# Optimization experiments

Hardware: AMD Instinct MI355X
Metric: run time of the kernel (lower is better)

Reference implementation:

```python
import jax, jax.numpy as jnp
import numpy as np

B, P, D, H, A, C = 256, 512, 16, 256, 8, 2
HID = 256
IN_MLP = H + A + 1  # 265


def setup_inputs() -> dict:
    key = jax.random.key(0)
    ks = jax.random.split(key, 12)
    s = 0.05  # small init for recurrent stability
    return {
        "particles": jax.random.normal(ks[0], (B, P, D), jnp.float32),
        "weights": jax.random.uniform(ks[1], (B, P), jnp.float32),
        "actions": jax.random.normal(ks[2], (B, A), jnp.float32),
        "time": jax.random.uniform(ks[3], (B,), jnp.float32) * 100.0,
        "Wi": jax.random.normal(ks[4], (D + 1, 3 * H), jnp.float32) * s,
        "bi": jnp.zeros((3 * H,), jnp.float32),
        "Wh_rz": jax.random.normal(ks[5], (H, 2 * H), jnp.float32) * s,
        "Wh_n": jax.random.normal(ks[6], (H, H), jnp.float32) * s,
        "bn": jnp.zeros((H,), jnp.float32),
        "mlp_W1": jax.random.normal(ks[7], (C, IN_MLP, HID), jnp.float32) * s,
        "mlp_b1": jnp.zeros((C, HID), jnp.float32),
        "mlp_W2": jax.random.normal(ks[8], (C, HID, HID), jnp.float32) * s,
        "mlp_b2": jnp.zeros((C, HID), jnp.float32),
        "mlp_W3": jax.random.normal(ks[9], (C, HID, 1), jnp.float32) * s,
        "mlp_b3": jnp.zeros((C, 1), jnp.float32),
        "num_time_steps": 100,
    }


def reference(particles, weights, actions, time, Wi, bi, Wh_rz, Wh_n, bn,
              mlp_W1, mlp_b1, mlp_W2, mlp_b2, mlp_W3, mlp_b3, num_time_steps):
    # feature_fn = identity; append weights as an extra feature channel
    x = jnp.concatenate([particles, weights[..., None]], axis=-1)  # [B, P, D+1]
    xs = jnp.swapaxes(x, 0, 1)  # [P, B, D+1], scan over particle axis

    def gru_step(h, xt):
        gi = xt @ Wi + bi  # [B, 3H]
        i_r, i_z, i_n = jnp.split(gi, 3, axis=-1)
        hrz = h @ Wh_rz  # [B, 2H], no bias (flax GRUCell hidden r/z dense)
        r = jax.nn.sigmoid(i_r + hrz[:, :H])
        z = jax.nn.sigmoid(i_z + hrz[:, H:])
        n = jnp.tanh(i_n + r * (h @ Wh_n + bn))
        h_new = (1.0 - z) * n + z * h
        return h_new, None

    h0 = jnp.zeros((particles.shape[0], H), particles.dtype)
    enc, _ = jax.lax.scan(gru_step, h0, xs)  # last hidden == take(outputs, -1, axis=-2)

    norm_time = time / num_time_steps
    hidden = jnp.concatenate([enc, actions, norm_time[..., None]], axis=-1)  # [B, IN_MLP]

    # n_critics MLPs evaluated batched over critic axis c
    h1 = jax.nn.relu(jnp.einsum('bi,cio->bco', hidden, mlp_W1) + mlp_b1)
    h2 = jax.nn.relu(jnp.einsum('bci,cio->bco', h1, mlp_W2) + mlp_b2)
    q = jnp.einsum('bci,cio->bco', h2, mlp_W3) + mlp_b3  # [B, C, 1]
    return q[..., 0]  # [B, C]
```

## Files before the change

### kernel.cpp

```cpp
#include <hip/hip_runtime.h>
#include <hip/hip_fp16.h>

typedef _Float16 h2v __attribute__((ext_vector_type(2)));
typedef _Float16 f16x8 __attribute__((ext_vector_type(8)));
typedef float f32x4 __attribute__((ext_vector_type(4)));
typedef unsigned int u32;
typedef unsigned short u16;

#define NB 256
#define NP 512
#define NH 256
#define NCOL 768

#define OFF_WH 0
#define LEN_WH 98304
#define OFF_WI (OFF_WH + LEN_WH)
#define LEN_WI 6912
#define OFF_W1 (OFF_WI + LEN_WI)
#define LEN_W1 68096
#define OFF_W2 (OFF_W1 + LEN_W1)
#define LEN_W2 65536
#define OFF_W3 (OFF_W2 + LEN_W2)
#define LEN_W3 256
#define WS_DWORDS (OFF_W3 + LEN_W3)

__device__ __forceinline__ u32 pack2(float lo, float hi) {
    h2v v; v.x = (_Float16)lo; v.y = (_Float16)hi;
    return __builtin_bit_cast(u32, v);
}

__device__ __forceinline__ float fdot2(u32 a, u32 b, float c) {
#if __has_builtin(__builtin_amdgcn_fdot2)
    return __builtin_amdgcn_fdot2(__builtin_bit_cast(h2v, a),
                                  __builtin_bit_cast(h2v, b), c, false);
#else
    h2v x = __builtin_bit_cast(h2v, a), y = __builtin_bit_cast(h2v, b);
    return c + (float)x.x * (float)y.x + (float)x.y * (float)y.y;
#endif
}

__global__ __launch_bounds__(256) void pack_kernel(
    const float* __restrict__ Wi, const float* __restrict__ Whrz,
    const float* __restrict__ Whn, const float* __restrict__ W1,
    const float* __restrict__ W2, const float* __restrict__ W3,
    u32* __restrict__ ws)
{
    for (int F = blockIdx.x * 256 + threadIdx.x; F < WS_DWORDS; F += gridDim.x * 256) {
        u32 val;
        if (F < OFF_WI) {
            int d = F & 3; int r = F >> 2;
            int l = r & 63; int q = r >> 6;
            int f = q % 48; int w = q / 48;
            int t = f >> 3; int kt = f & 7;
            int k = kt * 32 + ((l >> 4) << 3) + 2 * d;
            int col = w * 96 + t * 16 + (l & 15);
            float lo, hi;
            if (col < 512) { lo = Whrz[k * 512 + col]; hi = Whrz[(k + 1) * 512 + col]; }
            else { lo = Whn[k * 256 + (col - 512)]; hi = Whn[(k + 1) * 256 + (col - 512)]; }
            val = pack2(lo, hi);
        } else if (F < OFF_W1) {
            int j = F - OFF_WI; int kk = j / NCOL; int col = j % NCOL;
            int k = 2 * kk;
            float lo = Wi[k * NCOL + col];
            float hi = (k + 1 < 17) ? Wi[(k + 1) * NCOL + col] : 0.f;
            val = pack2(lo, hi);
        } else if (F < OFF_W2) {
            int j = F - OFF_W1; int c = j / (133 * 256); int r = j % (133 * 256);
            int kk = r >> 8; int o = r & 255;
            int k = 2 * kk;
            float lo = W1[(c * 265 + k) * 256 + o];
            float hi = (k + 1 < 265) ? W1[(c * 265 + k + 1) * 256 + o] : 0.f;
            val = pack2(lo, hi);
        } else if (F < OFF_W3) {
            int j = F - OFF_W2; int c = j >> 15; int r = j & 32767;
            int kk = r >> 8; int o = r & 255;
            float lo = W2[(c * 256 + 2 * kk) * 256 + o];
            float hi = W2[(c * 256 + 2 * kk + 1) * 256 + o];
            val = pack2(lo, hi);
        } else {
            int j = F - OFF_W3; int c = j >> 7; int jj = j & 127;
            float lo = W3[c * 256 + 2 * jj];
            float hi = W3[c * 256 + 2 * jj + 1];
            val = pack2(lo, hi);
        }
        ws[F] = val;
    }
}

__global__ __launch_bounds__(512, 2) void qnet_kernel(
    const float* __restrict__ particles, const float* __restrict__ pweights,
    const float* __restrict__ actions, const float* __restrict__ timev,
    const float* __restrict__ bi, const float* __restrict__ bn,
    const float* __restrict__ b1, const float* __restrict__ b2,
    const float* __restrict__ b3, const int* __restrict__ nts,
    const u32* __restrict__ ws, float* __restrict__ out)
{
    __shared__ __align__(16) u32 sWi[LEN_WI];
    __shared__ __align__(16) u32 sX[NP * 9];
    __shared__ __align__(16) float sCols[NCOL];
    __shared__ __align__(16) u32 sH2[NH / 2];
    __shared__ __align__(16) float sHf[NH];
    __shared__ __align__(16) float sMisc[16];

    u32* sHid = sWi;
    u16* sL1 = (u16*)sX;
    u16* sL2 = (u16*)sCols;

    const int b = blockIdx.x;
    const int tid = threadIdx.x;
    const int lane = tid & 63;
    const int wid = tid >> 6;

    f16x8 bf[48];
    {
        const uint4* gp = (const uint4*)(ws + OFF_WH) + (wid * 48) * 64 + lane;
        #pragma unroll
        for (int i = 0; i < 48; ++i) bf[i] = __builtin_bit_cast(f16x8, gp[i * 64]);
    }
    for (int j = tid; j < LEN_WI; j += 512) sWi[j] = ws[OFF_WI + j];
    {
        const float4* pr = (const float4*)(particles + (long)b * NP * 16);
        for (int j = tid; j < NP * 4; j += 512) {
            float4 v = pr[j];
            int p = j >> 2, d4 = j & 3;
            sX[p * 9 + d4 * 2]     = pack2(v.x, v.y);
            sX[p * 9 + d4 * 2 + 1] = pack2(v.z, v.w);
        }
        const float* wr = pweights + (long)b * NP;
        for (int p = tid; p < NP; p += 512) sX[p * 9 + 8] = pack2(wr[p], 0.f);
    }
    if (tid < NH / 2) sH2[tid] = 0u;
    if (tid < 8) sMisc[tid] = actions[b * 8 + tid];
    if (tid == 8) sMisc[8] = timev[b] / (float)nts[0];

    float hreg = 0.f, bir = 0.f, biz = 0.f, binn = 0.f, bnn = 0.f;
    if (tid < NH) {
        bir = bi[tid]; biz = bi[NH + tid]; binn = bi[2 * NH + tid]; bnn = bn[tid];
    }
    __syncthreads();

    const uint4* h4 = ((const uint4*)sH2) + (lane >> 4);
    float* colp = sCols + wid * 96 + (lane & 15);

    #pragma unroll 1
    for (int p = 0; p < NP; ++p) {
        f32x4 a0 = {0.f, 0.f, 0.f, 0.f}, a1 = a0, a2 = a0, a3 = a0, a4 = a0, a5 = a0;
        #pragma unroll
        for (int kt = 0; kt < 8; ++kt) {
            f16x8 av = __builtin_bit_cast(f16x8, h4[kt * 4]);
            a0 = __builtin_amdgcn_mfma_f32_16x16x32_f16(av, bf[kt],      a0, 0, 0, 0);
            a1 = __builtin_amdgcn_mfma_f32_16x16x32_f16(av, bf[8 + kt],  a1, 0, 0, 0);
            a2 = __builtin_amdgcn_mfma_f32_16x16x32_f16(av, bf[16 + kt], a2, 0, 0, 0);
            a3 = __builtin_amdgcn_mfma_f32_16x16x32_f16(av, bf[24 + kt], a3, 0, 0, 0);
            a4 = __builtin_amdgcn_mfma_f32_16x16x32_f16(av, bf[32 + kt], a4, 0, 0, 0);
            a5 = __builtin_amdgcn_mfma_f32_16x16x32_f16(av, bf[40 + kt], a5, 0, 0, 0);
        }

        float xr = 0.f, xz = 0.f, xn = 0.f;
        if (tid < NH) {
            xr = bir; xz = biz; xn = binn;
            const u32* xp = &sX[p * 9];
            #pragma unroll
            for (int kk = 0; kk < 9; ++kk) {
                u32 xv = xp[kk];
                xr = fdot2(sWi[kk * NCOL + tid], xv, xr);
                xz = fdot2(sWi[kk * NCOL + NH + tid], xv, xz);
                xn = fdot2(sWi[kk * NCOL + 2 * NH + tid], xv, xn);
            }
        }

        if (lane < 16) {
            colp[0]  = a0[0]; colp[16] = a1[0]; colp[32] = a2[0];
            colp[48] = a3[0]; colp[64] = a4[0]; colp[80] = a5[0];
        }
        __syncthreads();
        if (tid < NH) {
            float sr = sCols[tid];
            float sz = sCols[NH + tid];
            float sn = sCols[2 * NH + tid];
            float r = 1.f / (1.f + __expf(-(sr + xr)));
            float z = 1.f / (1.f + __expf(-(sz + xz)));
            float targ = xn + r * (sn + bnn);
            float e2 = __expf(2.f * targ);
            float n = 1.f - 2.f / (e2 + 1.f);
            hreg = (1.f - z) * n + z * hreg;
            _Float16 hh = (_Float16)hreg;
            ((u16*)sH2)[tid] = __builtin_bit_cast(u16, hh);
        }
        __syncthreads();
    }

    if (tid < NH) sHf[tid] = hreg;
    __syncthreads();
    if (tid < 128) sHid[tid] = pack2(sHf[2 * tid], sHf[2 * tid + 1]);
    else if (tid < 132) { int i = tid - 128; sHid[tid] = pack2(sMisc[2 * i], sMisc[2 * i + 1]); }
    else if (tid == 132) sHid[132] = pack2(sMisc[8], 0.f);
    __syncthreads();
    {
        int c = tid >> 8, o = tid & 255;
        float acc = b1[c * 256 + o];
        const u32* wp = ws + OFF_W1 + c * 133 * 256 + o;
        #pragma unroll 4
        for (int kk = 0; kk < 133; ++kk) acc = fdot2(wp[kk * 256], sHid[kk], acc);
        acc = fmaxf(acc, 0.f);
        _Float16 a16 = (_Float16)acc;
        sL1[tid] = __builtin_bit_cast(u16, a16);
    }
    __syncthreads();
    {
        int c = tid >> 8, o = tid & 255;
        float acc = b2[c * 256 + o];
        const u32* wp = ws + OFF_W2 + c * 128 * 256 + o;
        const u32* hp = (const u32*)sL1 + c * 128;
        #pragma unroll 4
        for (int kk = 0; kk < 128; ++kk) acc = fdot2(wp[kk * 256], hp[kk], acc);
        acc = fmaxf(acc, 0.f);
        _Float16 a16 = (_Float16)acc;
        sL2[tid] = __builtin_bit_cast(u16, a16);
    }
    __syncthreads();
    if (tid < 128) {
        int c = tid >> 6, l = tid & 63;
        const u32* wp = ws + OFF_W3 + c * 128;
        const u32* hp = (const u32*)sL2 + c * 128;
        float acc = fdot2(wp[l], hp[l], 0.f);
        acc = fdot2(wp[64 + l], hp[64 + l], acc);
        #pragma unroll
        for (int off = 32; off > 0; off >>= 1) acc += __shfl_down(acc, off);
        if (l == 0) out[b * 2 + c] = acc + b3[c];
    }
}

extern "C" void kernel_launch(void* const* d_in, const int* in_sizes, int n_in,
                              void* d_out, int out_size, void* d_ws, size_t ws_size,
                              hipStream_t stream) {
    const float* particles = (const float*)d_in[0];
    const float* pweights  = (const float*)d_in[1];
    const float* actions   = (const float*)d_in[2];
    const float* timev     = (const float*)d_in[3];
    const float* Wi        = (const float*)d_in[4];
    const float* bi        = (const float*)d_in[5];
    const float* Whrz      = (const float*)d_in[6];
    const float* Whn       = (const float*)d_in[7];
    const float* bn        = (const float*)d_in[8];
    const float* W1        = (const float*)d_in[9];
    const float* b1        = (const float*)d_in[10];
    const float* W2        = (const float*)d_in[11];
    const float* b2        = (const float*)d_in[12];
    const float* W3        = (const float*)d_in[13];
    const float* b3        = (const float*)d_in[14];
    const int*   nts       = (const int*)d_in[15];
    u32* ws = (u32*)d_ws;
    float* outp = (float*)d_out;

    pack_kernel<<<WS_DWORDS / 256, 256, 0, stream>>>(Wi, Whrz, Whn, W1, W2, W3, ws);
    qnet_kernel<<<NB, 512, 0, stream>>>(particles, pweights, actions, timev,
                                        bi, bn, b1, b2, b3, nts, ws, outp);
}
```

Before: 697.2 us.

## Batch input projection via MFMA every 16 steps and cut per-step barriers

The input projection x@Wi is now computed with MFMA for 16 particles at once and staged in shared memory, replacing the per-step fdot2 loop over sWi. The hidden-weight column layout is reordered so each wave owns 32 hidden units across r/z/n, letting lanes combine gates from their own MFMA accumulators without the sCols round trip. The hidden state is double-buffered, so each step needs one barrier instead of two. In exchange there is an extra barrier every 16 steps, more shared memory for sG, and only half of each wave's lanes do the gate math.

```diff
diff --git a/kernel.cpp b/kernel.cpp
--- a/kernel.cpp
+++ b/kernel.cpp
@@ -10,13 +10,12 @@
 #define NB 256
 #define NP 512
 #define NH 256
-#define NCOL 768
 
 #define OFF_WH 0
 #define LEN_WH 98304
-#define OFF_WI (OFF_WH + LEN_WH)
-#define LEN_WI 6912
-#define OFF_W1 (OFF_WI + LEN_WI)
+#define OFF_WIB (OFF_WH + LEN_WH)
+#define LEN_WIB 12288
+#define OFF_W1 (OFF_WIB + LEN_WIB)
 #define LEN_W1 68096
 #define OFF_W2 (OFF_W1 + LEN_W1)
 #define LEN_W2 65536
@@ -47,22 +46,28 @@
 {
     for (int F = blockIdx.x * 256 + threadIdx.x; F < WS_DWORDS; F += gridDim.x * 256) {
         u32 val;
-        if (F < OFF_WI) {
+        if (F < OFF_WIB) {
             int d = F & 3; int r = F >> 2;
             int l = r & 63; int q = r >> 6;
             int f = q % 48; int w = q / 48;
             int t = f >> 3; int kt = f & 7;
+            int g = t >> 1, c = t & 1;
             int k = kt * 32 + ((l >> 4) << 3) + 2 * d;
-            int col = w * 96 + t * 16 + (l & 15);
+            int col = g * 256 + w * 32 + c * 16 + (l & 15);
             float lo, hi;
             if (col < 512) { lo = Whrz[k * 512 + col]; hi = Whrz[(k + 1) * 512 + col]; }
             else { lo = Whn[k * 256 + (col - 512)]; hi = Whn[(k + 1) * 256 + (col - 512)]; }
             val = pack2(lo, hi);
         } else if (F < OFF_W1) {
-            int j = F - OFF_WI; int kk = j / NCOL; int col = j % NCOL;
-            int k = 2 * kk;
-            float lo = Wi[k * NCOL + col];
-            float hi = (k + 1 < 17) ? Wi[(k + 1) * NCOL + col] : 0.f;
+            int j = F - OFF_WIB;
+            int d = j & 3; int r = j >> 2;
+            int l = r & 63; int q = r >> 6;
+            int t = q % 6; int w = q / 6;
+            int g = t >> 1, c = t & 1;
+            int k = ((l >> 4) << 3) + 2 * d;
+            int col = g * 256 + w * 32 + c * 16 + (l & 15);
+            float lo = (k < 17) ? Wi[k * 768 + col] : 0.f;
+            float hi = (k + 1 < 17) ? Wi[(k + 1) * 768 + col] : 0.f;
             val = pack2(lo, hi);
         } else if (F < OFF_W2) {
             int j = F - OFF_W1; int c = j / (133 * 256); int r = j % (133 * 256);
@@ -95,103 +100,119 @@
     const float* __restrict__ b3, const int* __restrict__ nts,
     const u32* __restrict__ ws, float* __restrict__ out)
 {
-    __shared__ __align__(16) u32 sWi[LEN_WI];
-    __shared__ __align__(16) u32 sX[NP * 9];
-    __shared__ __align__(16) float sCols[NCOL];
-    __shared__ __align__(16) u32 sH2[NH / 2];
+    __shared__ __align__(16) u32 sX[NP * 16];
+    __shared__ __align__(16) float sG[8 * 1536];
+    __shared__ __align__(16) u32 sH2[2][128];
     __shared__ __align__(16) float sHf[NH];
     __shared__ __align__(16) float sMisc[16];
-
-    u32* sHid = sWi;
-    u16* sL1 = (u16*)sX;
-    u16* sL2 = (u16*)sCols;
 
     const int b = blockIdx.x;
     const int tid = threadIdx.x;
     const int lane = tid & 63;
     const int wid = tid >> 6;
 
-    f16x8 bf[48];
+    f16x8 bfh[48];
     {
         const uint4* gp = (const uint4*)(ws + OFF_WH) + (wid * 48) * 64 + lane;
         #pragma unroll
-        for (int i = 0; i < 48; ++i) bf[i] = __builtin_bit_cast(f16x8, gp[i * 64]);
-    }
-    for (int j = tid; j < LEN_WI; j += 512) sWi[j] = ws[OFF_WI + j];
-    {
-        const float4* pr = (const float4*)(particles + (long)b * NP * 16);
-        for (int j = tid; j < NP * 4; j += 512) {
-            float4 v = pr[j];
-            int p = j >> 2, d4 = j & 3;
-            sX[p * 9 + d4 * 2]     = pack2(v.x, v.y);
-            sX[p * 9 + d4 * 2 + 1] = pack2(v.z, v.w);
+        for (int i = 0; i < 48; ++i) bfh[i] = __builtin_bit_cast(f16x8, gp[i * 64]);
+    }
+    {
+        const float2* pr2 = (const float2*)(particles + (long)b * NP * 16);
+        for (int j = tid; j < NP * 8; j += 512) {
+            int p = j >> 3, q = j & 7;
+            float2 v = pr2[j];
+            sX[p * 16 + q] = pack2(v.x, v.y);
         }
         const float* wr = pweights + (long)b * NP;
-        for (int p = tid; p < NP; p += 512) sX[p * 9 + 8] = pack2(wr[p], 0.f);
-    }
-    if (tid < NH / 2) sH2[tid] = 0u;
+        for (int j = tid; j < NP * 8; j += 512) {
+            int p = j >> 3, q = j & 7;
+            sX[p * 16 + 8 + q] = (q == 0) ? pack2(wr[p], 0.f) : 0u;
+        }
+    }
+    if (tid < 256) ((u32*)sH2)[tid] = 0u;
     if (tid < 8) sMisc[tid] = actions[b * 8 + tid];
     if (tid == 8) sMisc[8] = timev[b] / (float)nts[0];
 
-    float hreg = 0.f, bir = 0.f, biz = 0.f, binn = 0.f, bnn = 0.f;
-    if (tid < NH) {
-        bir = bi[tid]; biz = bi[NH + tid]; binn = bi[2 * NH + tid]; bnn = bn[tid];
-    }
-    __syncthreads();
-
-    const uint4* h4 = ((const uint4*)sH2) + (lane >> 4);
-    float* colp = sCols + wid * 96 + (lane & 15);
+    float birL = 0.f, bizL = 0.f, binnL = 0.f, bnnL = 0.f, hreg = 0.f;
+    if (lane < 32) {
+        int j = wid * 32 + lane;
+        birL = bi[j]; bizL = bi[NH + j]; binnL = bi[2 * NH + j]; bnnL = bn[j];
+    }
+    __syncthreads();
+
+    const uint4* wibp = (const uint4*)(ws + OFF_WIB) + (wid * 6) * 64 + lane;
 
     #pragma unroll 1
     for (int p = 0; p < NP; ++p) {
+        if ((p & 15) == 0) {
+            f16x8 av = __builtin_bit_cast(f16x8,
+                ((const uint4*)sX)[(p + (lane & 15)) * 4 + (lane >> 4)]);
+            f32x4 z4 = {0.f, 0.f, 0.f, 0.f};
+            f32x4 g0 = __builtin_amdgcn_mfma_f32_16x16x32_f16(av, __builtin_bit_cast(f16x8, wibp[0 * 64]), z4, 0, 0, 0);
+            f32x4 g1 = __builtin_amdgcn_mfma_f32_16x16x32_f16(av, __builtin_bit_cast(f16x8, wibp[1 * 64]), z4, 0, 0, 0);
+            f32x4 g2 = __builtin_amdgcn_mfma_f32_16x16x32_f16(av, __builtin_bit_cast(f16x8, wibp[2 * 64]), z4, 0, 0, 0);
+            f32x4 g3 = __builtin_amdgcn_mfma_f32_16x16x32_f16(av, __builtin_bit_cast(f16x8, wibp[3 * 64]), z4, 0, 0, 0);
+            f32x4 g4 = __builtin_amdgcn_mfma_f32_16x16x32_f16(av, __builtin_bit_cast(f16x8, wibp[4 * 64]), z4, 0, 0, 0);
+            f32x4 g5 = __builtin_amdgcn_mfma_f32_16x16x32_f16(av, __builtin_bit_cast(f16x8, wibp[5 * 64]), z4, 0, 0, 0);
+            int sb = (lane >> 4) << 2;
+            float* gw = sG + wid * 1536 + (lane & 15);
+            #pragma unroll
+            for (int r = 0; r < 4; ++r) {
+                gw[(sb + r) * 32]          = g0[r];
+                gw[(sb + r) * 32 + 16]     = g1[r];
+                gw[512 + (sb + r) * 32]    = g2[r];
+                gw[512 + (sb + r) * 32 + 16] = g3[r];
+                gw[1024 + (sb + r) * 32]   = g4[r];
+                gw[1024 + (sb + r) * 32 + 16] = g5[r];
+            }
+            __syncthreads();
+        }
+
+        float gR = 0.f, gZ = 0.f, gN = 0.f;
+        {
+            const float* gp = sG + wid * 1536 + (p & 15) * 32 + (lane & 31);
+            gR = gp[0]; gZ = gp[512]; gN = gp[1024];
+        }
+
+        const u32* hbuf = sH2[p & 1];
         f32x4 a0 = {0.f, 0.f, 0.f, 0.f}, a1 = a0, a2 = a0, a3 = a0, a4 = a0, a5 = a0;
         #pragma unroll
         for (int kt = 0; kt < 8; ++kt) {
-            f16x8 av = __builtin_bit_cast(f16x8, h4[kt * 4]);
-            a0 = __builtin_amdgcn_mfma_f32_16x16x32_f16(av, bf[kt],      a0, 0, 0, 0);
-            a1 = __builtin_amdgcn_mfma_f32_16x16x32_f16(av, bf[8 + kt],  a1, 0, 0, 0);
-            a2 = __builtin_amdgcn_mfma_f32_16x16x32_f16(av, bf[16 + kt], a2, 0, 0, 0);
-            a3 = __builtin_amdgcn_mfma_f32_16x16x32_f16(av, bf[24 + kt], a3, 0, 0, 0);
-            a4 = __builtin_amdgcn_mfma_f32_16x16x32_f16(av, bf[32 + kt], a4, 0, 0, 0);
-            a5 = __builtin_amdgcn_mfma_f32_16x16x32_f16(av, bf[40 + kt], a5, 0, 0, 0);
-        }
-
-        float xr = 0.f, xz = 0.f, xn = 0.f;
-        if (tid < NH) {
-            xr = bir; xz = biz; xn = binn;
-            const u32* xp = &sX[p * 9];
-            #pragma unroll
-            for (int kk = 0; kk < 9; ++kk) {
-                u32 xv = xp[kk];
-                xr = fdot2(sWi[kk * NCOL + tid], xv, xr);
-                xz = fdot2(sWi[kk * NCOL + NH + tid], xv, xz);
-                xn = fdot2(sWi[kk * NCOL + 2 * NH + tid], xv, xn);
-            }
-        }
-
-        if (lane < 16) {
-            colp[0]  = a0[0]; colp[16] = a1[0]; colp[32] = a2[0];
-            colp[48] = a3[0]; colp[64] = a4[0]; colp[80] = a5[0];
-        }
-        __syncthreads();
-        if (tid < NH) {
-            float sr = sCols[tid];
-            float sz = sCols[NH + tid];
-            float sn = sCols[2 * NH + tid];
-            float r = 1.f / (1.f + __expf(-(sr + xr)));
-            float z = 1.f / (1.f + __expf(-(sz + xz)));
-            float targ = xn + r * (sn + bnn);
+            f16x8 hv = __builtin_bit_cast(f16x8, ((const uint4*)hbuf)[kt * 4 + (lane >> 4)]);
+            a0 = __builtin_amdgcn_mfma_f32_16x16x32_f16(hv, bfh[kt],      a0, 0, 0, 0);
+            a1 = __builtin_amdgcn_mfma_f32_16x16x32_f16(hv, bfh[8 + kt],  a1, 0, 0, 0);
+            a2 = __builtin_amdgcn_mfma_f32_16x16x32_f16(hv, bfh[16 + kt], a2, 0, 0, 0);
+            a3 = __builtin_amdgcn_mfma_f32_16x16x32_f16(hv, bfh[24 + kt], a3, 0, 0, 0);
+            a4 = __builtin_amdgcn_mfma_f32_16x16x32_f16(hv, bfh[32 + kt], a4, 0, 0, 0);
+            a5 = __builtin_amdgcn_mfma_f32_16x16x32_f16(hv, bfh[40 + kt], a5, 0, 0, 0);
+        }
+
+        bool hic = (lane & 16) != 0;
+        float srm = hic ? a1[0] : a0[0];
+        float szm = hic ? a3[0] : a2[0];
+        float snm = hic ? a5[0] : a4[0];
+        if (lane < 32) {
+            float xr = gR + birL + srm;
+            float xz = gZ + bizL + szm;
+            float xn = gN + binnL;
+            float r = 1.f / (1.f + __expf(-xr));
+            float z = 1.f / (1.f + __expf(-xz));
+            float targ = xn + r * (snm + bnnL);
             float e2 = __expf(2.f * targ);
             float n = 1.f - 2.f / (e2 + 1.f);
             hreg = (1.f - z) * n + z * hreg;
             _Float16 hh = (_Float16)hreg;
-            ((u16*)sH2)[tid] = __builtin_bit_cast(u16, hh);
+            ((u16*)sH2[(p + 1) & 1])[wid * 32 + lane] = __builtin_bit_cast(u16, hh);
         }
         __syncthreads();
     }
 
-    if (tid < NH) sHf[tid] = hreg;
-    __syncthreads();
+    if (lane < 32) sHf[wid * 32 + lane] = hreg;
+    __syncthreads();
+    u32* sHid = (u32*)sG;
+    u16* sL1 = (u16*)(sG + 512);
+    u16* sL2 = (u16*)(sG + 1024);
     if (tid < 128) sHid[tid] = pack2(sHf[2 * tid], sHf[2 * tid + 1]);
     else if (tid < 132) { int i = tid - 128; sHid[tid] = pack2(sMisc[2 * i], sMisc[2 * i + 1]); }
     else if (tid == 132) sHid[132] = pack2(sMisc[8], 0.f);
@@ -253,7 +274,7 @@
     u32* ws = (u32*)d_ws;
     float* outp = (float*)d_out;
 
-    pack_kernel<<<WS_DWORDS / 256, 256, 0, stream>>>(Wi, Whrz, Whn, W1, W2, W3, ws);
+    pack_kernel<<<(WS_DWORDS + 255) / 256, 256, 0, stream>>>(Wi, Whrz, Whn, W1, W2, W3, ws);
     qnet_kernel<<<NB, 512, 0, stream>>>(particles, pweights, actions, timev,
                                         bi, bn, b1, b2, b3, nts, ws, outp);
 }
```

Measured after the change: 629.6 us. -9.7%, faster.
